# Kernel tuning notes

Hardware: AMD Instinct MI355X
Metric: run time of the kernel (lower is better)

## Reference

```python
import jax, jax.numpy as jnp
import numpy as np

DIM = 128
H = 4            # num_heads
HD = DIM // H    # head_dim = 32
NH = H // 2      # half heads
MAXD = 128       # rpe max_dist
SPAN = 2 * MAXD + 1
TABLE = SPAN * SPAN
LAMBDA_INIT = 0.8


def setup_inputs() -> dict:
    key = jax.random.key(0)
    ks = jax.random.split(key, 18)
    B, Nq, Nkv = 2, 2048, 4096
    n = jax.random.normal
    inp = {
        "x_q": n(ks[0], (B, Nq, DIM), dtype=jnp.float32),
        "x_kv": n(ks[1], (B, Nkv, DIM), dtype=jnp.float32),
        "coords_q": jax.random.randint(ks[2], (B, Nq, 2), 0, 256, dtype=jnp.int32),
        "coords_k": jax.random.randint(ks[3], (B, Nkv, 2), 0, 256, dtype=jnp.int32),
        "alpha_map": jax.random.uniform(ks[4], (B, Nq, 1), dtype=jnp.float32),
        # projection weights stored input-major: y = x @ W + b
        "Wq": n(ks[5], (DIM, DIM), dtype=jnp.float32) * 0.02,
        "bq": jnp.zeros((DIM,), jnp.float32),
        "Wk": n(ks[6], (DIM, DIM), dtype=jnp.float32) * 0.02,
        "bk": jnp.zeros((DIM,), jnp.float32),
        "Wv": n(ks[7], (DIM, DIM), dtype=jnp.float32) * 0.02,
        "bv": jnp.zeros((DIM,), jnp.float32),
        "lq1": n(ks[8], (NH, HD), dtype=jnp.float32) * 0.1,
        "lk1": n(ks[9], (NH, HD), dtype=jnp.float32) * 0.1,
        "lq2": n(ks[10], (NH, HD), dtype=jnp.float32) * 0.1,
        "lk2": n(ks[11], (NH, HD), dtype=jnp.float32) * 0.1,
        "rpe_table": n(ks[12], (TABLE, H), dtype=jnp.float32) * 0.02,
        "Wp": n(ks[13], (DIM, DIM), dtype=jnp.float32) * 0.02,
        "bp": jnp.zeros((DIM,), jnp.float32),
    }
    return inp


def reference(x_q, x_kv, coords_q, coords_k, alpha_map,
              Wq, bq, Wk, bk, Wv, bv,
              lq1, lk1, lq2, lk2, rpe_table, Wp, bp):
    B, Nq, C = x_q.shape
    Nkv = x_kv.shape[1]
    scale = HD ** -0.5

    def to_heads(x, W, b, n):
        return (x @ W + b).reshape(B, n, H, HD).transpose(0, 2, 1, 3)  # [B,H,n,hd]

    q = to_heads(x_q, Wq, bq, Nq)
    k = to_heads(x_kv, Wk, bk, Nkv)
    v = to_heads(x_kv, Wv, bv, Nkv)

    # relative position bias gather: [B,Nq,Nkv] indices into [TABLE,H]
    rel = coords_q[:, :, None, :] - coords_k[:, None, :, :] + MAXD
    rel = jnp.clip(rel, 0, 2 * MAXD)
    idx = rel[..., 0] * SPAN + rel[..., 1]
    bias = jnp.transpose(rpe_table[idx], (0, 3, 1, 2))  # [B,H,Nq,Nkv]

    scores = jnp.einsum('bhqd,bhkd->bhqk', q, k) * scale + bias
    probs = jax.nn.softmax(scores, axis=-1)
    x_std = jnp.einsum('bhqk,bhkd->bhqd', probs, v)

    lam = (jnp.exp(jnp.sum(lq1 * lk1, axis=-1))
           - jnp.exp(jnp.sum(lq2 * lk2, axis=-1)) + LAMBDA_INIT)  # [NH]
    attn_diff = probs[:, :NH] - lam[None, :, None, None] * probs[:, NH:]
    x_diff = jnp.einsum('bhqk,bhkd->bhqd', attn_diff, v[:, :NH])

    x1 = x_std[:, :NH] + alpha_map[:, None, :, :] * x_diff  # alpha gating
    x = jnp.concatenate([x1, x_std[:, NH:]], axis=1)        # [B,H,Nq,hd]
    x = x.transpose(0, 2, 1, 3).reshape(B, Nq, C)
    return x @ Wp + bp
```

## Files before the change

### kernel.cpp

```cpp
#include <hip/hip_runtime.h>
#include <hip/hip_bf16.h>

#define B_ 2
#define H_ 4
#define HD_ 32
#define NQ_ 2048
#define NKV_ 4096
#define DIM_ 128
#define SPAN_ 257
#define SCALE_ 0.17677669529663687f
#define LAMBDA_INIT_ 0.8f
#define DTHR 4.0f

typedef float f32x4 __attribute__((ext_vector_type(4)));
typedef short s16x4 __attribute__((ext_vector_type(4)));
typedef short s16x8 __attribute__((ext_vector_type(8)));
typedef int   i32x4 __attribute__((ext_vector_type(4)));
typedef float fl4   __attribute__((ext_vector_type(4)));

static __device__ __forceinline__ unsigned short f2bf(float f) {
  unsigned u = __float_as_uint(f);
  u += 0x7FFFu + ((u >> 16) & 1u);
  return (unsigned short)(u >> 16);
}
static __device__ __forceinline__ unsigned cvtpk(float lo, float hi) {
  unsigned r;
  asm("v_cvt_pk_bf16_f32 %0, %1, %2" : "=v"(r) : "v"(lo), "v"(hi));
  return r;
}

__global__ __launch_bounds__(256) void qkv8(
    const float* __restrict__ xq, const float* __restrict__ xkv,
    const float* __restrict__ Wq, const float* __restrict__ bq,
    const float* __restrict__ Wk, const float* __restrict__ bk,
    const float* __restrict__ Wv, const float* __restrict__ bv,
    unsigned short* __restrict__ Qb, unsigned short* __restrict__ Kb,
    unsigned short* __restrict__ Vsw) {
  const int idx = blockIdx.x;
  const bool isq = idx < 512;
  const int b  = isq ? (idx >> 8) : ((idx - 512) >> 9);
  const int n0 = isq ? ((idx & 255) * 8) : (((idx - 512) & 511) * 8);
  const float* xsrc = isq ? xq : xkv;
  const int nlen = isq ? NQ_ : NKV_;

  __shared__ __align__(16) float xr[8][DIM_];
  const int tid = threadIdx.x;
  {
    const float* xbase = xsrc + ((size_t)b * nlen + n0) * DIM_;
    int rr = tid >> 5, c4 = tid & 31;
    *(fl4*)&xr[rr][c4 * 4] = *(const fl4*)(xbase + rr * DIM_ + c4 * 4);
  }
  __syncthreads();

  if (isq) {
    const int j = tid & 127, rh = tid >> 7;
    float acc[4];
    float bb = bq[j];
#pragma unroll
    for (int rr = 0; rr < 4; ++rr) acc[rr] = bb;
    for (int i4 = 0; i4 < 32; ++i4) {
      const float* wp = &Wq[(4 * i4) * DIM_ + j];
      float w0 = wp[0], w1 = wp[DIM_], w2 = wp[2 * DIM_], w3 = wp[3 * DIM_];
#pragma unroll
      for (int rr = 0; rr < 4; ++rr) {
        fl4 x4 = *(const fl4*)&xr[4 * rh + rr][4 * i4];
        acc[rr] = fmaf(x4[3], w3, fmaf(x4[2], w2, fmaf(x4[1], w1, fmaf(x4[0], w0, acc[rr]))));
      }
    }
    int h = j >> 5, d = j & 31;
    unsigned short* qb = Qb + (((size_t)b * H_ + h) * NQ_ + n0 + 4 * rh) * HD_ + d;
#pragma unroll
    for (int rr = 0; rr < 4; ++rr) qb[rr * HD_] = f2bf(acc[rr]);
  } else {
    const int half = tid >> 7, j = tid & 127;
    const float* W = half ? Wv : Wk;
    float bb = half ? bv[j] : bk[j];
    float acc[8];
#pragma unroll
    for (int rr = 0; rr < 8; ++rr) acc[rr] = bb;
    for (int i4 = 0; i4 < 32; ++i4) {
      const float* wp = &W[(4 * i4) * DIM_ + j];
      float w0 = wp[0], w1 = wp[DIM_], w2 = wp[2 * DIM_], w3 = wp[3 * DIM_];
#pragma unroll
      for (int rr = 0; rr < 8; ++rr) {
        fl4 x4 = *(const fl4*)&xr[rr][4 * i4];
        acc[rr] = fmaf(x4[3], w3, fmaf(x4[2], w2, fmaf(x4[1], w1, fmaf(x4[0], w0, acc[rr]))));
      }
    }
    int h = j >> 5, d = j & 31;
    if (half == 0) {
      unsigned short* kb2 = Kb + (((size_t)b * H_ + h) * NKV_ + n0) * HD_ + d;
#pragma unroll
      for (int rr = 0; rr < 8; ++rr) kb2[rr * HD_] = f2bf(acc[rr]);
    } else {
      unsigned short* vb = Vsw + (((size_t)b * H_ + h) * HD_ + d) * NKV_ + (n0 & ~31);
      const int base = n0 & 31;
#pragma unroll
      for (int c = 0; c < 2; ++c) {
        int k0r = base + 4 * c;
        int posb = (k0r < 16) ? 8 * (k0r >> 2) : 8 * ((k0r - 16) >> 2) + 4;
        s16x4 t4;
#pragma unroll
        for (int e = 0; e < 4; ++e) t4[e] = (short)f2bf(acc[4 * c + e]);
        *(s16x4*)(vb + posb) = t4;
      }
    }
  }
}

__global__ __launch_bounds__(512) void attn_nb(
    const unsigned short* __restrict__ Qg, const unsigned short* __restrict__ Kg,
    const unsigned short* __restrict__ Vg, const int* __restrict__ cq,
    const int* __restrict__ ck, const float* __restrict__ alpha,
    const float* __restrict__ rpe, const float* __restrict__ lq1,
    const float* __restrict__ lk1, const float* __restrict__ lq2,
    const float* __restrict__ lk2, const float* __restrict__ Wp,
    const float* __restrict__ bp, float* __restrict__ out) {

  const int tid = threadIdx.x;
  const int lane = tid & 63;
  const int wv = tid >> 6;
  const int qcol = lane & 15;
  const int g = lane >> 4;
  const int qt = blockIdx.x & 127;
  const int b = blockIdx.x >> 7;
  const int qg0 = qt * 16;
  const int k_base = wv * 512;

  __shared__ struct {
    union {
      float acc[3][8][16][36];
      float xq[16][128];
    } u;
    float mW[8][17];
    float lW[4][8][17];
    float wgt[8][17];
    float lam[2];
  } S;

  if (tid < 2) {
    float s1 = 0.f, s2 = 0.f;
    for (int d = 0; d < HD_; ++d) {
      s1 += lq1[tid * HD_ + d] * lk1[tid * HD_ + d];
      s2 += lq2[tid * HD_ + d] * lk2[tid * HD_ + d];
    }
    S.lam[tid] = __expf(s1) - __expf(s2) + LAMBDA_INIT_;
  }

  s16x8 qf[4];
#pragma unroll
  for (int h = 0; h < 4; ++h)
    qf[h] = *(const s16x8*)(Qg + (((size_t)b * H_ + h) * NQ_ + qg0 + qcol) * HD_ + 8 * g);

  const int2 cqv = ((const int2*)cq)[(size_t)b * NQ_ + qg0 + qcol];
  const int qx = cqv.x + 128, qy = cqv.y + 128;

  const unsigned short* kb[4];
  const unsigned short* vp[4][2];
#pragma unroll
  for (int h = 0; h < 4; ++h) {
    kb[h] = Kg + (((size_t)b * H_ + h) * NKV_ + k_base) * HD_;
#pragma unroll
    for (int dt = 0; dt < 2; ++dt)
      vp[h][dt] = Vg + (((size_t)b * H_ + h) * HD_ + dt * 16 + qcol) * NKV_ + k_base + 8 * g;
  }
  int koff[2];
#pragma unroll
  for (int t = 0; t < 2; ++t) koff[t] = (16 * t + qcol) * HD_ + 8 * g;

  const i32x4* ck4 = (const i32x4*)ck + (((size_t)b * NKV_ + k_base) >> 1);
  const fl4* __restrict__ rpe4 = (const fl4*)rpe;

  float m_run = -INFINITY;
  float l_run[4] = {0.f, 0.f, 0.f, 0.f};
  f32x4 z4 = {0.f, 0.f, 0.f, 0.f};
  f32x4 aS[4][2], aC[2][2];
#pragma unroll
  for (int h = 0; h < 4; ++h) { aS[h][0] = z4; aS[h][1] = z4; }
#pragma unroll
  for (int p = 0; p < 2; ++p) { aC[p][0] = z4; aC[p][1] = z4; }

  s16x8 kf[4][2], vf[4][2];
  i32x4 ckt[4];
  fl4 gB[8];

#define CKLD(ST) {                                                         \
    const int s_ = (ST);                                                   \
    _Pragma("unroll") for (int t = 0; t < 2; ++t)                          \
    _Pragma("unroll") for (int hf = 0; hf < 2; ++hf)                       \
      ckt[2 * t + hf] = ck4[s_ * 16 + 8 * t + 2 * g + hf];                 \
  }
#define KLD(ST) {                                                          \
    const int s_ = (ST);                                                   \
    _Pragma("unroll") for (int h = 0; h < 4; ++h)                          \
    _Pragma("unroll") for (int t = 0; t < 2; ++t)                          \
      kf[h][t] = *(const s16x8*)(kb[h] + s_ * 32 * HD_ + koff[t]);         \
  }
#define VLD(ST) {                                                          \
    const int s_ = (ST);                                                   \
    _Pragma("unroll") for (int h = 0; h < 4; ++h)                          \
    _Pragma("unroll") for (int dt = 0; dt < 2; ++dt)                       \
      vf[h][dt] = *(const s16x8*)(vp[h][dt] + s_ * 32);                    \
  }
#define GATH() {                                                           \
    _Pragma("unroll") for (int t = 0; t < 2; ++t)                          \
    _Pragma("unroll") for (int hf = 0; hf < 2; ++hf) {                     \
      i32x4 cc = ckt[2 * t + hf];                                          \
      int dx0 = qx - cc[0]; dx0 = dx0 < 0 ? 0 : (dx0 > 256 ? 256 : dx0);   \
      int dy0 = qy - cc[1]; dy0 = dy0 < 0 ? 0 : (dy0 > 256 ? 256 : dy0);   \
      gB[4 * t + 2 * hf] = rpe4[dx0 * SPAN_ + dy0];                        \
      int dx1 = qx - cc[2]; dx1 = dx1 < 0 ? 0 : (dx1 > 256 ? 256 : dx1);   \
      int dy1 = qy - cc[3]; dy1 = dy1 < 0 ? 0 : (dy1 > 256 ? 256 : dy1);   \
      gB[4 * t + 2 * hf + 1] = rpe4[dx1 * SPAN_ + dy1];                    \
    }                                                                      \
  }

  CKLD(0);
  KLD(0);
  GATH();
  CKLD(1);

  for (int st = 0; st < 16; ++st) {
    f32x4 s0[4], s1[4];
#pragma unroll
    for (int h = 0; h < 4; ++h) {
      s0[h] = __builtin_amdgcn_mfma_f32_16x16x32_bf16(kf[h][0], qf[h], z4, 0, 0, 0);
      s1[h] = __builtin_amdgcn_mfma_f32_16x16x32_bf16(kf[h][1], qf[h], z4, 0, 0, 0);
    }
    VLD(st);
    KLD(st + 1 < 16 ? st + 1 : 15);

    float sv[4][8];
    float mx = -INFINITY;
#pragma unroll
    for (int h = 0; h < 4; ++h) {
#pragma unroll
      for (int r = 0; r < 4; ++r) {
        sv[h][r]     = fmaf(s0[h][r], SCALE_, gB[r][h]);
        sv[h][4 + r] = fmaf(s1[h][r], SCALE_, gB[4 + r][h]);
        mx = fmaxf(mx, fmaxf(sv[h][r], sv[h][4 + r]));
      }
    }
    mx = fmaxf(mx, __shfl_xor(mx, 16));
    mx = fmaxf(mx, __shfl_xor(mx, 32));
    if (__any(mx > m_run + DTHR)) {
      float mnew = fmaxf(m_run, mx);
      float fold = __expf(m_run - mnew);
      float fr[4];
#pragma unroll
      for (int r = 0; r < 4; ++r) fr[r] = __shfl(fold, 4 * g + r);
#pragma unroll
      for (int h = 0; h < 4; ++h) {
        l_run[h] *= fold;
#pragma unroll
        for (int dt = 0; dt < 2; ++dt)
#pragma unroll
          for (int r = 0; r < 4; ++r) aS[h][dt][r] *= fr[r];
      }
#pragma unroll
      for (int p = 0; p < 2; ++p)
#pragma unroll
        for (int dt = 0; dt < 2; ++dt)
#pragma unroll
          for (int r = 0; r < 4; ++r) aC[p][dt][r] *= fr[r];
      m_run = mnew;
    }
    s16x8 pa[4];
#pragma unroll
    for (int h = 0; h < 4; ++h) {
      float p[8], psum = 0.f;
#pragma unroll
      for (int s = 0; s < 8; ++s) { p[s] = __expf(sv[h][s] - m_run); psum += p[s]; }
      l_run[h] += psum;
      i32x4 pw;
#pragma unroll
      for (int c = 0; c < 4; ++c) pw[c] = (int)cvtpk(p[2 * c], p[2 * c + 1]);
      pa[h] = __builtin_bit_cast(s16x8, pw);
    }
    GATH();
    CKLD(st + 2 < 16 ? st + 2 : 15);

#pragma unroll
    for (int h = 0; h < 4; ++h)
#pragma unroll
      for (int dt = 0; dt < 2; ++dt)
        aS[h][dt] = __builtin_amdgcn_mfma_f32_16x16x32_bf16(pa[h], vf[h][dt], aS[h][dt], 0, 0, 0);
#pragma unroll
    for (int p = 0; p < 2; ++p)
#pragma unroll
      for (int dt = 0; dt < 2; ++dt)
        aC[p][dt] = __builtin_amdgcn_mfma_f32_16x16x32_bf16(pa[p + 2], vf[p][dt], aC[p][dt], 0, 0, 0);
  }

#pragma unroll
  for (int h = 0; h < 4; ++h) {
    l_run[h] += __shfl_xor(l_run[h], 16);
    l_run[h] += __shfl_xor(l_run[h], 32);
  }
  if (lane < 16) {
    S.mW[wv][lane] = m_run;
#pragma unroll
    for (int h = 0; h < 4; ++h) S.lW[h][wv][lane] = l_run[h];
  }
  __syncthreads();
  if (tid < 128) {
    int w = tid >> 4, q = tid & 15;
    float M = -INFINITY;
#pragma unroll
    for (int w2 = 0; w2 < 8; ++w2) M = fmaxf(M, S.mW[w2][q]);
    S.wgt[w][q] = __expf(S.mW[w][q] - M);
  }
  __syncthreads();

#pragma unroll
  for (int p = 0; p < 3; ++p)
#pragma unroll
    for (int dt = 0; dt < 2; ++dt)
#pragma unroll
      for (int r = 0; r < 4; ++r)
        S.u.acc[p][wv][4 * g + r][dt * 16 + qcol] = aS[p][dt][r];
  __syncthreads();
  const int q = tid >> 5, d = tid & 31;
  float wg[8];
#pragma unroll
  for (int w = 0; w < 8; ++w) wg[w] = S.wgt[w][q];
  float sumA[3] = {0.f, 0.f, 0.f};
#pragma unroll
  for (int p = 0; p < 3; ++p)
#pragma unroll
    for (int w = 0; w < 8; ++w) sumA[p] = fmaf(wg[w], S.u.acc[p][w][q][d], sumA[p]);
  __syncthreads();

#pragma unroll
  for (int dt = 0; dt < 2; ++dt)
#pragma unroll
    for (int r = 0; r < 4; ++r) {
      S.u.acc[0][wv][4 * g + r][dt * 16 + qcol] = aS[3][dt][r];
      S.u.acc[1][wv][4 * g + r][dt * 16 + qcol] = aC[0][dt][r];
      S.u.acc[2][wv][4 * g + r][dt * 16 + qcol] = aC[1][dt][r];
    }
  __syncthreads();
  float sumB[3] = {0.f, 0.f, 0.f};
#pragma unroll
  for (int p = 0; p < 3; ++p)
#pragma unroll
    for (int w = 0; w < 8; ++w) sumB[p] = fmaf(wg[w], S.u.acc[p][w][q][d], sumB[p]);

  float L[4];
#pragma unroll
  for (int h = 0; h < 4; ++h) {
    float s = 0.f;
#pragma unroll
    for (int w = 0; w < 8; ++w) s = fmaf(S.lW[h][w][q], S.wgt[w][q], s);
    L[h] = s;
  }
  float a = alpha[(size_t)b * NQ_ + qg0 + q];
  float lam0 = S.lam[0], lam1 = S.lam[1];
  float xv0 = (1.f + a) * sumA[0] / L[0] - a * lam0 * sumB[1] / L[2];
  float xv1 = (1.f + a) * sumA[1] / L[1] - a * lam1 * sumB[2] / L[3];
  float xv2 = sumA[2] / L[2];
  float xv3 = sumB[0] / L[3];

  __syncthreads();
  S.u.xq[q][d]      = xv0;
  S.u.xq[q][32 + d] = xv1;
  S.u.xq[q][64 + d] = xv2;
  S.u.xq[q][96 + d] = xv3;
  __syncthreads();

  {
    const int j = tid & 127, rg = tid >> 7;
    float ob[4];
    float bpj = bp[j];
#pragma unroll
    for (int rr = 0; rr < 4; ++rr) ob[rr] = bpj;
#pragma unroll 4
    for (int i = 0; i < DIM_; ++i) {
      float w = Wp[i * DIM_ + j];
#pragma unroll
      for (int rr = 0; rr < 4; ++rr) ob[rr] = fmaf(S.u.xq[4 * rg + rr][i], w, ob[rr]);
    }
#pragma unroll
    for (int rr = 0; rr < 4; ++rr)
      out[((size_t)b * NQ_ + qg0 + 4 * rg + rr) * DIM_ + j] = ob[rr];
  }
}

extern "C" void kernel_launch(void* const* d_in, const int* in_sizes, int n_in,
                              void* d_out, int out_size, void* d_ws, size_t ws_size,
                              hipStream_t stream) {
  const float* x_q   = (const float*)d_in[0];
  const float* x_kv  = (const float*)d_in[1];
  const int*   cq    = (const int*)d_in[2];
  const int*   ckc   = (const int*)d_in[3];
  const float* alpha = (const float*)d_in[4];
  const float* Wq    = (const float*)d_in[5];
  const float* bq    = (const float*)d_in[6];
  const float* Wk    = (const float*)d_in[7];
  const float* bk    = (const float*)d_in[8];
  const float* Wv    = (const float*)d_in[9];
  const float* bv    = (const float*)d_in[10];
  const float* lq1   = (const float*)d_in[11];
  const float* lk1   = (const float*)d_in[12];
  const float* lq2   = (const float*)d_in[13];
  const float* lk2   = (const float*)d_in[14];
  const float* rpe   = (const float*)d_in[15];
  const float* Wp    = (const float*)d_in[16];
  const float* bp    = (const float*)d_in[17];
  float* out = (float*)d_out;

  char* w = (char*)d_ws;
  unsigned short* Qb  = (unsigned short*)w;
  unsigned short* Kb  = (unsigned short*)(w + 1048576);
  unsigned short* Vsw = (unsigned short*)(w + 3145728);

  qkv8<<<dim3(1536), dim3(256), 0, stream>>>(
      x_q, x_kv, Wq, bq, Wk, bk, Wv, bv, Qb, Kb, Vsw);

  attn_nb<<<dim3(B_ * (NQ_ / 16)), dim3(512), 0, stream>>>(
      Qb, Kb, Vsw, cq, ckc, alpha, rpe, lq1, lk1, lq2, lk2, Wp, bp, out);
}
```

Measured before the change: 113.7 us.

## Sort queries and keys by x-coordinate and stage RPE window in shared memory

Adds a prep kernel that counting-sorts query and key coordinates by x and converts the RPE table to packed bf16. Q, K and V are written in sorted order. Each attention block then loads the band of RPE rows reachable by its sorted 16-query tile and the current 256-key stage into LDS, and gathers bias from there, falling back to the global fp32 table outside the band. This is meant to replace scattered global gathers with LDS reads, at the cost of an extra kernel launch, per-stage syncs and window loads, and scattered permuted writes. Bias values read from the window are rounded to bf16.

Measured after the change: 127.8 us. 1.12x slower.

```diff
diff --git a/kernel.cpp b/kernel.cpp
--- a/kernel.cpp
+++ b/kernel.cpp
@@ -8,9 +8,11 @@
 #define NKV_ 4096
 #define DIM_ 128
 #define SPAN_ 257
+#define TABLE_ 66049
 #define SCALE_ 0.17677669529663687f
 #define LAMBDA_INIT_ 0.8f
 #define DTHR 4.0f
+#define CAPR 36
 
 typedef float f32x4 __attribute__((ext_vector_type(4)));
 typedef short s16x4 __attribute__((ext_vector_type(4)));
@@ -29,11 +31,93 @@
   return r;
 }
 
-__global__ __launch_bounds__(256) void qkv8(
+__global__ __launch_bounds__(256) void prep(
+    const int* __restrict__ cq, const int* __restrict__ ck,
+    const float* __restrict__ rpe,
+    int* __restrict__ cqs, int* __restrict__ cks,
+    int* __restrict__ qperm, int* __restrict__ kperm,
+    int* __restrict__ qrank, int* __restrict__ krank,
+    uint2* __restrict__ rpeb) {
+  const int tid = threadIdx.x;
+  const int blk = blockIdx.x;
+  if (blk >= 4) {
+    int ci = (blk - 4) * 256 + tid;
+    if (ci < TABLE_) {
+      fl4 v = *(const fl4*)(rpe + 4 * ci);
+      uint2 o;
+      o.x = cvtpk(v[0], v[1]);
+      o.y = cvtpk(v[2], v[3]);
+      rpeb[ci] = o;
+    }
+    return;
+  }
+  const int b = blk >> 1;
+  const bool isq = (blk & 1) == 0;
+  const int N = isq ? NQ_ : NKV_;
+  const int S = N >> 8;
+  const int* src = (isq ? cq : ck) + b * N * 2;
+  int* sc   = (isq ? cqs : cks) + b * N * 2;
+  int* perm = (isq ? qperm : kperm) + b * N;
+  int* rank = (isq ? qrank : krank) + b * N;
+
+  __shared__ int xv[NKV_];
+  __shared__ int hist[16][256];
+  __shared__ int wavehist[4][256];
+  __shared__ int pref[256];
+
+  for (int i = tid; i < N; i += 256) xv[i] = src[2 * i];
+  for (int i = tid; i < S * 256; i += 256) ((int*)hist)[i] = 0;
+  __syncthreads();
+  for (int s = 0; s < S; ++s) atomicAdd(&hist[s][xv[s * 256 + tid]], 1);
+  __syncthreads();
+  int tot = 0;
+  for (int s = 0; s < S; ++s) tot += hist[s][tid];
+  pref[tid] = tot;
+  __syncthreads();
+  if (tid == 0) {
+    int run = 0;
+    for (int i = 0; i < 256; ++i) { int t = pref[i]; pref[i] = run; run += t; }
+  }
+  __syncthreads();
+  {
+    int run = pref[tid];
+    for (int s = 0; s < S; ++s) { int h = hist[s][tid]; hist[s][tid] = run; run += h; }
+  }
+  const int lane = tid & 63, w = tid >> 6;
+  __syncthreads();
+  for (int s = 0; s < S; ++s) {
+    wavehist[w][lane] = 0; wavehist[w][64 + lane] = 0;
+    wavehist[w][128 + lane] = 0; wavehist[w][192 + lane] = 0;
+    int e = s * 256 + tid;
+    int x = xv[e];
+    unsigned long long m = ~0ull;
+#pragma unroll
+    for (int bit = 0; bit < 8; ++bit) {
+      unsigned long long bl = __ballot((x >> bit) & 1);
+      m &= ((x >> bit) & 1) ? bl : ~bl;
+    }
+    unsigned long long lt = (1ull << lane) - 1ull;
+    int lrank = __popcll(m & lt);
+    if ((m & lt) == 0ull) wavehist[w][x] = __popcll(m);
+    __syncthreads();
+    int offs = 0;
+#pragma unroll
+    for (int w2 = 0; w2 < 4; ++w2) if (w2 < w) offs += wavehist[w2][x];
+    int r = hist[s][x] + offs + lrank;
+    perm[r] = e;
+    rank[e] = r;
+    sc[2 * r] = x;
+    sc[2 * r + 1] = src[2 * e + 1];
+    __syncthreads();
+  }
+}
+
+__global__ __launch_bounds__(256) void qkv8p(
     const float* __restrict__ xq, const float* __restrict__ xkv,
     const float* __restrict__ Wq, const float* __restrict__ bq,
     const float* __restrict__ Wk, const float* __restrict__ bk,
     const float* __restrict__ Wv, const float* __restrict__ bv,
+    const int* __restrict__ qrank, const int* __restrict__ krank,
     unsigned short* __restrict__ Qb, unsigned short* __restrict__ Kb,
     unsigned short* __restrict__ Vsw) {
   const int idx = blockIdx.x;
@@ -68,9 +152,11 @@
       }
     }
     int h = j >> 5, d = j & 31;
-    unsigned short* qb = Qb + (((size_t)b * H_ + h) * NQ_ + n0 + 4 * rh) * HD_ + d;
-#pragma unroll
-    for (int rr = 0; rr < 4; ++rr) qb[rr * HD_] = f2bf(acc[rr]);
+#pragma unroll
+    for (int rr = 0; rr < 4; ++rr) {
+      int rq = qrank[b * NQ_ + n0 + 4 * rh + rr];
+      Qb[(((size_t)b * H_ + h) * NQ_ + rq) * HD_ + d] = f2bf(acc[rr]);
+    }
   } else {
     const int half = tid >> 7, j = tid & 127;
     const float* W = half ? Wv : Wk;
@@ -89,33 +175,34 @@
     }
     int h = j >> 5, d = j & 31;
     if (half == 0) {
-      unsigned short* kb2 = Kb + (((size_t)b * H_ + h) * NKV_ + n0) * HD_ + d;
-#pragma unroll
-      for (int rr = 0; rr < 8; ++rr) kb2[rr * HD_] = f2bf(acc[rr]);
+#pragma unroll
+      for (int rr = 0; rr < 8; ++rr) {
+        int rk = krank[b * NKV_ + n0 + rr];
+        Kb[(((size_t)b * H_ + h) * NKV_ + rk) * HD_ + d] = f2bf(acc[rr]);
+      }
     } else {
-      unsigned short* vb = Vsw + (((size_t)b * H_ + h) * HD_ + d) * NKV_ + (n0 & ~31);
-      const int base = n0 & 31;
-#pragma unroll
-      for (int c = 0; c < 2; ++c) {
-        int k0r = base + 4 * c;
-        int posb = (k0r < 16) ? 8 * (k0r >> 2) : 8 * ((k0r - 16) >> 2) + 4;
-        s16x4 t4;
-#pragma unroll
-        for (int e = 0; e < 4; ++e) t4[e] = (short)f2bf(acc[4 * c + e]);
-        *(s16x4*)(vb + posb) = t4;
+#pragma unroll
+      for (int rr = 0; rr < 8; ++rr) {
+        int rk = krank[b * NKV_ + n0 + rr];
+        int blk32 = rk & ~31, j32 = rk & 31;
+        int posb = (j32 < 16) ? 8 * (j32 >> 2) + (j32 & 3)
+                              : 8 * ((j32 - 16) >> 2) + 4 + (j32 & 3);
+        Vsw[(((size_t)b * H_ + h) * HD_ + d) * NKV_ + blk32 + posb] = f2bf(acc[rr]);
       }
     }
   }
 }
 
-__global__ __launch_bounds__(512) void attn_nb(
+__global__ __launch_bounds__(512) void attn_win(
     const unsigned short* __restrict__ Qg, const unsigned short* __restrict__ Kg,
-    const unsigned short* __restrict__ Vg, const int* __restrict__ cq,
-    const int* __restrict__ ck, const float* __restrict__ alpha,
-    const float* __restrict__ rpe, const float* __restrict__ lq1,
-    const float* __restrict__ lk1, const float* __restrict__ lq2,
-    const float* __restrict__ lk2, const float* __restrict__ Wp,
-    const float* __restrict__ bp, float* __restrict__ out) {
+    const unsigned short* __restrict__ Vg, const int* __restrict__ cqs,
+    const int* __restrict__ cks, const int* __restrict__ qperm,
+    const float* __restrict__ alpha, const uint2* __restrict__ rpeb,
+    const float* __restrict__ rpe,
+    const float* __restrict__ lq1, const float* __restrict__ lk1,
+    const float* __restrict__ lq2, const float* __restrict__ lk2,
+    const float* __restrict__ Wp, const float* __restrict__ bp,
+    float* __restrict__ out) {
 
   const int tid = threadIdx.x;
   const int lane = tid & 63;
@@ -125,12 +212,12 @@
   const int qt = blockIdx.x & 127;
   const int b = blockIdx.x >> 7;
   const int qg0 = qt * 16;
-  const int k_base = wv * 512;
 
   __shared__ struct {
     union {
       float acc[3][8][16][36];
       float xq[16][128];
+      uint2 wnd[CAPR * 257];
     } u;
     float mW[8][17];
     float lW[4][8][17];
@@ -152,23 +239,27 @@
   for (int h = 0; h < 4; ++h)
     qf[h] = *(const s16x8*)(Qg + (((size_t)b * H_ + h) * NQ_ + qg0 + qcol) * HD_ + 8 * g);
 
-  const int2 cqv = ((const int2*)cq)[(size_t)b * NQ_ + qg0 + qcol];
+  const int2* cq2 = (const int2*)cqs + (size_t)b * NQ_;
+  const int2* ck2 = (const int2*)cks + (size_t)b * NKV_;
+  const int2 cqv = cq2[qg0 + qcol];
   const int qx = cqv.x + 128, qy = cqv.y + 128;
+  const int qxminp = cq2[qg0].x + 128;
+  const int qxmaxp = cq2[qg0 + 15].x + 128;
 
   const unsigned short* kb[4];
   const unsigned short* vp[4][2];
 #pragma unroll
   for (int h = 0; h < 4; ++h) {
-    kb[h] = Kg + (((size_t)b * H_ + h) * NKV_ + k_base) * HD_;
+    kb[h] = Kg + (((size_t)b * H_ + h) * NKV_ + wv * 32) * HD_;
 #pragma unroll
     for (int dt = 0; dt < 2; ++dt)
-      vp[h][dt] = Vg + (((size_t)b * H_ + h) * HD_ + dt * 16 + qcol) * NKV_ + k_base + 8 * g;
+      vp[h][dt] = Vg + (((size_t)b * H_ + h) * HD_ + dt * 16 + qcol) * NKV_ + wv * 32 + 8 * g;
   }
   int koff[2];
 #pragma unroll
   for (int t = 0; t < 2; ++t) koff[t] = (16 * t + qcol) * HD_ + 8 * g;
 
-  const i32x4* ck4 = (const i32x4*)ck + (((size_t)b * NKV_ + k_base) >> 1);
+  const i32x4* ck4 = (const i32x4*)cks + (((size_t)b * NKV_ + wv * 32) >> 1);
   const fl4* __restrict__ rpe4 = (const fl4*)rpe;
 
   float m_run = -INFINITY;
@@ -188,47 +279,68 @@
     const int s_ = (ST);                                                   \
     _Pragma("unroll") for (int t = 0; t < 2; ++t)                          \
     _Pragma("unroll") for (int hf = 0; hf < 2; ++hf)                       \
-      ckt[2 * t + hf] = ck4[s_ * 16 + 8 * t + 2 * g + hf];                 \
+      ckt[2 * t + hf] = ck4[s_ * 128 + 8 * t + 2 * g + hf];                \
   }
 #define KLD(ST) {                                                          \
     const int s_ = (ST);                                                   \
     _Pragma("unroll") for (int h = 0; h < 4; ++h)                          \
     _Pragma("unroll") for (int t = 0; t < 2; ++t)                          \
-      kf[h][t] = *(const s16x8*)(kb[h] + s_ * 32 * HD_ + koff[t]);         \
+      kf[h][t] = *(const s16x8*)(kb[h] + s_ * 256 * HD_ + koff[t]);        \
   }
 #define VLD(ST) {                                                          \
     const int s_ = (ST);                                                   \
     _Pragma("unroll") for (int h = 0; h < 4; ++h)                          \
     _Pragma("unroll") for (int dt = 0; dt < 2; ++dt)                       \
-      vf[h][dt] = *(const s16x8*)(vp[h][dt] + s_ * 32);                    \
-  }
-#define GATH() {                                                           \
+      vf[h][dt] = *(const s16x8*)(vp[h][dt] + s_ * 256);                   \
+  }
+#define LGATH(DXLO, RR) {                                                  \
     _Pragma("unroll") for (int t = 0; t < 2; ++t)                          \
     _Pragma("unroll") for (int hf = 0; hf < 2; ++hf) {                     \
       i32x4 cc = ckt[2 * t + hf];                                          \
-      int dx0 = qx - cc[0]; dx0 = dx0 < 0 ? 0 : (dx0 > 256 ? 256 : dx0);   \
-      int dy0 = qy - cc[1]; dy0 = dy0 < 0 ? 0 : (dy0 > 256 ? 256 : dy0);   \
-      gB[4 * t + 2 * hf] = rpe4[dx0 * SPAN_ + dy0];                        \
-      int dx1 = qx - cc[2]; dx1 = dx1 < 0 ? 0 : (dx1 > 256 ? 256 : dx1);   \
-      int dy1 = qy - cc[3]; dy1 = dy1 < 0 ? 0 : (dy1 > 256 ? 256 : dy1);   \
-      gB[4 * t + 2 * hf + 1] = rpe4[dx1 * SPAN_ + dy1];                    \
+      _Pragma("unroll") for (int e = 0; e < 2; ++e) {                      \
+        int dx = qx - cc[2 * e];     dx = dx < 0 ? 0 : (dx > 256 ? 256 : dx); \
+        int dy = qy - cc[2 * e + 1]; dy = dy < 0 ? 0 : (dy > 256 ? 256 : dy); \
+        int wr = dx - (DXLO);                                              \
+        fl4 gg;                                                            \
+        if (wr >= 0 && wr < (RR)) {                                        \
+          uint2 wd = S.u.wnd[wr * 257 + dy];                               \
+          gg[0] = __uint_as_float(wd.x << 16);                             \
+          gg[1] = __uint_as_float(wd.x & 0xffff0000u);                     \
+          gg[2] = __uint_as_float(wd.y << 16);                             \
+          gg[3] = __uint_as_float(wd.y & 0xffff0000u);                     \
+        } else {                                                           \
+          gg = rpe4[dx * SPAN_ + dy];                                      \
+        }                                                                  \
+        gB[4 * t + 2 * hf + e] = gg;                                       \
+      }                                                                    \
     }                                                                      \
   }
 
   CKLD(0);
   KLD(0);
-  GATH();
-  CKLD(1);
-
-  for (int st = 0; st < 16; ++st) {
+
+  for (int s = 0; s < 16; ++s) {
+    int2 kmn = ck2[s * 256];
+    int2 kmx = ck2[s * 256 + 255];
+    int dxlo = qxminp - kmx.x; dxlo = dxlo < 0 ? 0 : (dxlo > 256 ? 256 : dxlo);
+    int dxhi = qxmaxp - kmn.x; dxhi = dxhi < 0 ? 0 : (dxhi > 256 ? 256 : dxhi);
+    int R = dxhi - dxlo + 1; if (R > CAPR) R = CAPR;
+    __syncthreads();
+    for (int i = tid; i < R * 257; i += 512) {
+      int r = i / 257;
+      S.u.wnd[i] = rpeb[(dxlo + r) * 257 + (i - r * 257)];
+    }
+    __syncthreads();
+
     f32x4 s0[4], s1[4];
 #pragma unroll
     for (int h = 0; h < 4; ++h) {
       s0[h] = __builtin_amdgcn_mfma_f32_16x16x32_bf16(kf[h][0], qf[h], z4, 0, 0, 0);
       s1[h] = __builtin_amdgcn_mfma_f32_16x16x32_bf16(kf[h][1], qf[h], z4, 0, 0, 0);
     }
-    VLD(st);
-    KLD(st + 1 < 16 ? st + 1 : 15);
+    VLD(s);
+    KLD(s + 1 < 16 ? s + 1 : 15);
+    LGATH(dxlo, R);
 
     float sv[4][8];
     float mx = -INFINITY;
@@ -270,15 +382,14 @@
     for (int h = 0; h < 4; ++h) {
       float p[8], psum = 0.f;
 #pragma unroll
-      for (int s = 0; s < 8; ++s) { p[s] = __expf(sv[h][s] - m_run); psum += p[s]; }
+      for (int ss = 0; ss < 8; ++ss) { p[ss] = __expf(sv[h][ss] - m_run); psum += p[ss]; }
       l_run[h] += psum;
       i32x4 pw;
 #pragma unroll
       for (int c = 0; c < 4; ++c) pw[c] = (int)cvtpk(p[2 * c], p[2 * c + 1]);
       pa[h] = __builtin_bit_cast(s16x8, pw);
     }
-    GATH();
-    CKLD(st + 2 < 16 ? st + 2 : 15);
+    CKLD(s + 1 < 16 ? s + 1 : 15);
 
 #pragma unroll
     for (int h = 0; h < 4; ++h)
@@ -349,12 +460,13 @@
   float L[4];
 #pragma unroll
   for (int h = 0; h < 4; ++h) {
-    float s = 0.f;
-#pragma unroll
-    for (int w = 0; w < 8; ++w) s = fmaf(S.lW[h][w][q], S.wgt[w][q], s);
-    L[h] = s;
-  }
-  float a = alpha[(size_t)b * NQ_ + qg0 + q];
+    float ssum = 0.f;
+#pragma unroll
+    for (int w = 0; w < 8; ++w) ssum = fmaf(S.lW[h][w][q], S.wgt[w][q], ssum);
+    L[h] = ssum;
+  }
+  int aorig = qperm[b * NQ_ + qg0 + q];
+  float a = alpha[(size_t)b * NQ_ + aorig];
   float lam0 = S.lam[0], lam1 = S.lam[1];
   float xv0 = (1.f + a) * sumA[0] / L[0] - a * lam0 * sumB[1] / L[2];
   float xv1 = (1.f + a) * sumA[1] / L[1] - a * lam1 * sumB[2] / L[3];
@@ -381,8 +493,10 @@
       for (int rr = 0; rr < 4; ++rr) ob[rr] = fmaf(S.u.xq[4 * rg + rr][i], w, ob[rr]);
     }
 #pragma unroll
-    for (int rr = 0; rr < 4; ++rr)
-      out[((size_t)b * NQ_ + qg0 + 4 * rg + rr) * DIM_ + j] = ob[rr];
+    for (int rr = 0; rr < 4; ++rr) {
+      int orow = qperm[b * NQ_ + qg0 + 4 * rg + rr];
+      out[((size_t)b * NQ_ + orow) * DIM_ + j] = ob[rr];
+    }
   }
 }
 
@@ -410,13 +524,24 @@
   float* out = (float*)d_out;
 
   char* w = (char*)d_ws;
-  unsigned short* Qb  = (unsigned short*)w;
-  unsigned short* Kb  = (unsigned short*)(w + 1048576);
-  unsigned short* Vsw = (unsigned short*)(w + 3145728);
-
-  qkv8<<<dim3(1536), dim3(256), 0, stream>>>(
-      x_q, x_kv, Wq, bq, Wk, bk, Wv, bv, Qb, Kb, Vsw);
-
-  attn_nb<<<dim3(B_ * (NQ_ / 16)), dim3(512), 0, stream>>>(
-      Qb, Kb, Vsw, cq, ckc, alpha, rpe, lq1, lk1, lq2, lk2, Wp, bp, out);
+  unsigned short* Qb   = (unsigned short*)w;
+  unsigned short* Kb   = (unsigned short*)(w + 1048576);
+  unsigned short* Vsw  = (unsigned short*)(w + 3145728);
+  uint2*          rpeb = (uint2*)(w + 5242880);
+  int* cqs   = (int*)(w + 6291456);
+  int* cks   = (int*)(w + 6356992);
+  int* qperm = (int*)(w + 6422528);
+  int* kperm = (int*)(w + 6488064);
+  int* qrank = (int*)(w + 6553600);
+  int* krank = (int*)(w + 6619136);
+
+  prep<<<dim3(263), dim3(256), 0, stream>>>(
+      cq, ckc, rpe, cqs, cks, qperm, kperm, qrank, krank, rpeb);
+
+  qkv8p<<<dim3(1536), dim3(256), 0, stream>>>(
+      x_q, x_kv, Wq, bq, Wk, bk, Wv, bv, qrank, krank, Qb, Kb, Vsw);
+
+  attn_win<<<dim3(B_ * (NQ_ / 16)), dim3(512), 0, stream>>>(
+      Qb, Kb, Vsw, cqs, cks, qperm, alpha, rpeb, rpe,
+      lq1, lk1, lq2, lk2, Wp, bp, out);
 }
```
